# Performance work log

Measured on AMD Instinct MI355X. Metric: run time of the kernel, lower is better.

Reference implementation:

```python
import jax, jax.numpy as jnp
import numpy as np

B = 1048576  # batch size
D = 16       # in_dim == hid_dim == out_dim (required by the torch matmul broadcasting)


def setup_inputs() -> dict:
    key = jax.random.key(0)
    kx, kw = jax.random.split(key)
    x = jax.random.normal(kx, (B, D), dtype=jnp.float32)
    W = jax.random.normal(kw, (D, D, D), dtype=jnp.float32) * (1.0 / D)
    return {"x": x, "W": W}


def reference(x, W):
    # Original torch: xBx = x @ W @ x.T permuted, then take the batch diagonal.
    # Mathematically: out[b, k] = sum_{i, j} x[b, i] * W[k, i, j] * x[b, j]
    # (batched bilinear/quadratic form per output channel k). We compute only
    # the needed diagonal terms instead of the full BxB cross-batch product.
    return jnp.einsum('bi,kij,bj->bk', x, W, x)
```

## Files before the change

### kernel.cpp

```cpp
#include <hip/hip_runtime.h>
#include <hip/hip_bf16.h>


typedef __attribute__((ext_vector_type(8)))  short  short8;
typedef __attribute__((ext_vector_type(8)))  __bf16 bf16x8;
typedef __attribute__((ext_vector_type(4)))  float  floatx4;

#define DEV static __device__ __forceinline__

constexpr int cA(int c) {
    if (c < 24) { const int dIdx = c >> 1, v = c & 1;
        const int hi = dIdx / 3, lo = dIdx % 3 + 1;
        const int base = (hi == 3) ? 1 : 0;
        const int l = v ? ((lo == 1) ? 2 : 1) : 0;
        return base * 4 + l; }
    if (c < 36) { const int g = c - 24, hi = g / 4 + 1, l = g & 3;
        const int base = (hi == 3) ? 1 : 0;
        return base * 4 + l; }
    return c - 36;
}
constexpr int cDd(int c) {
    if (c < 24) { const int dIdx = c >> 1;
        return (dIdx / 3) * 4 + (dIdx % 3 + 1); }
    if (c < 36) { return ((c - 24) / 4 + 1) * 4; }
    return 0;
}
constexpr int   cB(int c) { return cA(c) ^ cDd(c); }
constexpr float cW(int c) { return (c >= 24 && c < 36) ? 0.5f : 1.0f; }

template <int C>
DEV float pval(const float* xv) {
    return xv[cA(C)] * xv[cB(C)];
}

template <int S>
DEV short8 make_afrag(const float* xv) {
    union { short8 s; __hip_bfloat162 h[4]; } u;
    u.h[0] = __float22bfloat162_rn(make_float2(pval<8 * S + 0>(xv), pval<8 * S + 1>(xv)));
    u.h[1] = __float22bfloat162_rn(make_float2(pval<8 * S + 2>(xv), pval<8 * S + 3>(xv)));
    u.h[2] = __float22bfloat162_rn(make_float2(pval<8 * S + 4>(xv), pval<8 * S + 5>(xv)));
    u.h[3] = __float22bfloat162_rn(make_float2(pval<8 * S + 6>(xv), pval<8 * S + 7>(xv)));
    return u.s;
}

DEV floatx4 mfma_bf16(short8 a, short8 b, floatx4 c) {
    return __builtin_amdgcn_mfma_f32_16x16x32_bf16(
        __builtin_bit_cast(bf16x8, a), __builtin_bit_cast(bf16x8, b), c, 0, 0, 0);
}

DEV float q_elem(const float* __restrict__ W, int e) {
    const int n = e / 160;
    const int k = e - n * 160;
    const int s = k >> 5, q = (k >> 3) & 3, j = k & 7;
    const int c = 8 * s + j;
    const int I = cA(c) ^ (q << 2);
    const int J = cB(c) ^ (q << 2);
    return (I == J) ? W[n * 256 + I * 16 + I]
                    : cW(c) * (W[n * 256 + I * 16 + J] + W[n * 256 + J * 16 + I]);
}

__global__ __launch_bounds__(256, 8)
void bilinear16_kernel(const float* __restrict__ x, const float* __restrict__ W,
                       float* __restrict__ out, int ntiles) {
    __shared__ __align__(16) short Qt[16][160];
    __shared__ __align__(16) float Tb[4][320];

    const int tid = threadIdx.x;
    for (int e = tid; e < 16 * 160; e += 256) {
        __hip_bfloat16 h = __float2bfloat16(q_elem(W, e));
        Qt[0][e] = *reinterpret_cast<short*>(&h);
    }
    __syncthreads();

    const int lane = tid & 63;
    const int n    = lane & 15;
    const int q    = lane >> 4;
    float* const tb = Tb[tid >> 6];

    short8 b0 = *reinterpret_cast<const short8*>(&Qt[n][0 * 32 + q * 8]);
    short8 b1 = *reinterpret_cast<const short8*>(&Qt[n][1 * 32 + q * 8]);
    short8 b2 = *reinterpret_cast<const short8*>(&Qt[n][2 * 32 + q * 8]);
    short8 b3 = *reinterpret_cast<const short8*>(&Qt[n][3 * 32 + q * 8]);
    short8 b4 = *reinterpret_cast<const short8*>(&Qt[n][4 * 32 + q * 8]);
    asm("" : "+a"(b0));
    asm("" : "+a"(b1));
    asm("" : "+a"(b2));
    asm("" : "+a"(b3));
    asm("" : "+a"(b4));

    const int waveId = blockIdx.x * 4 + (tid >> 6);
    const int nwaves = gridDim.x * 4;

    for (int t = waveId; t < ntiles; t += nwaves) {
        const float4 own = *reinterpret_cast<const float4*>(
            x + (size_t)t * 256 + n * 16 + q * 4);
        float4 s1, s2;
        s1.x = __shfl_xor(own.x, 16); s1.y = __shfl_xor(own.y, 16);
        s1.z = __shfl_xor(own.z, 16); s1.w = __shfl_xor(own.w, 16);
        s2.x = __shfl_xor(own.x, 32); s2.y = __shfl_xor(own.y, 32);
        s2.z = __shfl_xor(own.z, 32); s2.w = __shfl_xor(own.w, 32);
        const float xv[12] = {own.x, own.y, own.z, own.w,
                              s1.x,  s1.y,  s1.z,  s1.w,
                              s2.x,  s2.y,  s2.z,  s2.w};

        floatx4 acc0 = {0.f, 0.f, 0.f, 0.f};
        floatx4 acc1 = {0.f, 0.f, 0.f, 0.f};
        acc0 = mfma_bf16(make_afrag<0>(xv), b0, acc0);
        acc1 = mfma_bf16(make_afrag<1>(xv), b1, acc1);
        acc0 = mfma_bf16(make_afrag<2>(xv), b2, acc0);
        acc1 = mfma_bf16(make_afrag<3>(xv), b3, acc1);
        acc0 = mfma_bf16(make_afrag<4>(xv), b4, acc0);
        acc0 = acc0 + acc1;

        tb[(q * 4 + 0) * 20 + n] = acc0[0];
        tb[(q * 4 + 1) * 20 + n] = acc0[1];
        tb[(q * 4 + 2) * 20 + n] = acc0[2];
        tb[(q * 4 + 3) * 20 + n] = acc0[3];
        const float4 o = *reinterpret_cast<const float4*>(
            &tb[(lane >> 2) * 20 + (lane & 3) * 4]);
        *reinterpret_cast<float4*>(out + (size_t)t * 256 + lane * 4) = o;
    }
}

extern "C" void kernel_launch(void* const* d_in, const int* in_sizes, int n_in,
                              void* d_out, int out_size, void* d_ws, size_t ws_size,
                              hipStream_t stream) {
    const float* x = (const float*)d_in[0];
    const float* W = (const float*)d_in[1];
    float* out = (float*)d_out;
    const int Bn = in_sizes[0] / 16;
    const int ntiles = Bn >> 4;
    bilinear16_kernel<<<2048, 256, 0, stream>>>(x, W, out, ntiles);
}
```

Baseline: 122.9 us.

## Double-buffer x tiles into LDS via async global_load_lds prefetch

Adds a per-wave two-slot LDS ring filled with global_load_lds direct-to-LDS loads, so the loads for tile t+2 are in flight while tile t is computed. The loop is fully unrolled for the case of exactly 8 tiles per wave, which matches the default size (65536 tiles, 8192 waves). The ring also replaces the cross-lane shuffles: each lane reads its neighbours' x values straight from LDS. This is meant to hide global load latency in a memory-bound kernel, at the cost of extra LDS usage, manual vmcnt waits and a specialised code path that only fires when the tile count matches exactly.

```diff
diff --git a/kernel.cpp b/kernel.cpp
--- a/kernel.cpp
+++ b/kernel.cpp
@@ -59,11 +59,15 @@
                     : cW(c) * (W[n * 256 + I * 16 + J] + W[n * 256 + J * 16 + I]);
 }
 
+typedef const __attribute__((address_space(1))) unsigned char* gptr_t;
+typedef       __attribute__((address_space(3))) unsigned char* lptr_t;
+
 __global__ __launch_bounds__(256, 8)
 void bilinear16_kernel(const float* __restrict__ x, const float* __restrict__ W,
                        float* __restrict__ out, int ntiles) {
     __shared__ __align__(16) short Qt[16][160];
     __shared__ __align__(16) float Tb[4][320];
+    __shared__ __align__(16) float Ring[4][2][256];
 
     const int tid = threadIdx.x;
     for (int e = tid; e < 16 * 160; e += 256) {
@@ -75,34 +79,29 @@
     const int lane = tid & 63;
     const int n    = lane & 15;
     const int q    = lane >> 4;
-    float* const tb = Tb[tid >> 6];
+    const int wid  = tid >> 6;
+    float* const tb   = Tb[wid];
+    float* const ring = &Ring[wid][0][0];
 
     short8 b0 = *reinterpret_cast<const short8*>(&Qt[n][0 * 32 + q * 8]);
     short8 b1 = *reinterpret_cast<const short8*>(&Qt[n][1 * 32 + q * 8]);
     short8 b2 = *reinterpret_cast<const short8*>(&Qt[n][2 * 32 + q * 8]);
     short8 b3 = *reinterpret_cast<const short8*>(&Qt[n][3 * 32 + q * 8]);
     short8 b4 = *reinterpret_cast<const short8*>(&Qt[n][4 * 32 + q * 8]);
-    asm("" : "+a"(b0));
-    asm("" : "+a"(b1));
-    asm("" : "+a"(b2));
-    asm("" : "+a"(b3));
-    asm("" : "+a"(b4));
+    asm("" : "+a"(b0)); asm("" : "+a"(b1)); asm("" : "+a"(b2));
+    asm("" : "+a"(b3)); asm("" : "+a"(b4));
 
-    const int waveId = blockIdx.x * 4 + (tid >> 6);
+    const int waveId = blockIdx.x * 4 + wid;
     const int nwaves = gridDim.x * 4;
+    const int n16    = n * 16;
 
-    for (int t = waveId; t < ntiles; t += nwaves) {
-        const float4 own = *reinterpret_cast<const float4*>(
-            x + (size_t)t * 256 + n * 16 + q * 4);
-        float4 s1, s2;
-        s1.x = __shfl_xor(own.x, 16); s1.y = __shfl_xor(own.y, 16);
-        s1.z = __shfl_xor(own.z, 16); s1.w = __shfl_xor(own.w, 16);
-        s2.x = __shfl_xor(own.x, 32); s2.y = __shfl_xor(own.y, 32);
-        s2.z = __shfl_xor(own.z, 32); s2.w = __shfl_xor(own.w, 32);
-        const float xv[12] = {own.x, own.y, own.z, own.w,
-                              s1.x,  s1.y,  s1.z,  s1.w,
-                              s2.x,  s2.y,  s2.z,  s2.w};
-
+    auto tile_compute = [&](const float* rs, float* obase) {
+        const float4 v0 = *reinterpret_cast<const float4*>(rs + n16 + q * 4);
+        const float4 v1 = *reinterpret_cast<const float4*>(rs + n16 + (q ^ 1) * 4);
+        const float4 v2 = *reinterpret_cast<const float4*>(rs + n16 + (q ^ 2) * 4);
+        const float xv[12] = {v0.x, v0.y, v0.z, v0.w,
+                              v1.x, v1.y, v1.z, v1.w,
+                              v2.x, v2.y, v2.z, v2.w};
         floatx4 acc0 = {0.f, 0.f, 0.f, 0.f};
         floatx4 acc1 = {0.f, 0.f, 0.f, 0.f};
         acc0 = mfma_bf16(make_afrag<0>(xv), b0, acc0);
@@ -111,15 +110,64 @@
         acc1 = mfma_bf16(make_afrag<3>(xv), b3, acc1);
         acc0 = mfma_bf16(make_afrag<4>(xv), b4, acc0);
         acc0 = acc0 + acc1;
-
         tb[(q * 4 + 0) * 20 + n] = acc0[0];
         tb[(q * 4 + 1) * 20 + n] = acc0[1];
         tb[(q * 4 + 2) * 20 + n] = acc0[2];
         tb[(q * 4 + 3) * 20 + n] = acc0[3];
         const float4 o = *reinterpret_cast<const float4*>(
             &tb[(lane >> 2) * 20 + (lane & 3) * 4]);
-        *reinterpret_cast<float4*>(out + (size_t)t * 256 + lane * 4) = o;
+        *reinterpret_cast<float4*>(obase + lane * 4) = o;
+    };
+
+#define PREF(J)                                                                 \
+    __builtin_amdgcn_global_load_lds(                                           \
+        (gptr_t)(const void*)(x + (size_t)(t0 + (J) * nwaves) * 256 + lane * 4),\
+        (lptr_t)(void*)(ring + ((J) & 1) * 256), 16, 0, 0)
+
+#define TILE(J, VMC)                                                            \
+    do {                                                                        \
+        asm volatile("s_waitcnt vmcnt(" #VMC ")" ::: "memory");                 \
+        tile_compute(ring + ((J) & 1) * 256,                                    \
+                     out + (size_t)(t0 + (J) * nwaves) * 256);                  \
+        if ((J) < 6) { asm volatile("" ::: "memory"); PREF((J) + 2); }          \
+    } while (0)
+
+    if (ntiles == nwaves * 8) {
+        const int t0 = waveId;
+        PREF(0); PREF(1);
+        TILE(0, 1); TILE(1, 2); TILE(2, 2); TILE(3, 2);
+        TILE(4, 2); TILE(5, 2); TILE(6, 2); TILE(7, 1);
+    } else {
+        for (int t = waveId; t < ntiles; t += nwaves) {
+            const float4 own = *reinterpret_cast<const float4*>(
+                x + (size_t)t * 256 + n * 16 + q * 4);
+            float4 s1, s2;
+            s1.x = __shfl_xor(own.x, 16); s1.y = __shfl_xor(own.y, 16);
+            s1.z = __shfl_xor(own.z, 16); s1.w = __shfl_xor(own.w, 16);
+            s2.x = __shfl_xor(own.x, 32); s2.y = __shfl_xor(own.y, 32);
+            s2.z = __shfl_xor(own.z, 32); s2.w = __shfl_xor(own.w, 32);
+            const float xv[12] = {own.x, own.y, own.z, own.w,
+                                  s1.x,  s1.y,  s1.z,  s1.w,
+                                  s2.x,  s2.y,  s2.z,  s2.w};
+            floatx4 acc0 = {0.f, 0.f, 0.f, 0.f};
+            floatx4 acc1 = {0.f, 0.f, 0.f, 0.f};
+            acc0 = mfma_bf16(make_afrag<0>(xv), b0, acc0);
+            acc1 = mfma_bf16(make_afrag<1>(xv), b1, acc1);
+            acc0 = mfma_bf16(make_afrag<2>(xv), b2, acc0);
+            acc1 = mfma_bf16(make_afrag<3>(xv), b3, acc1);
+            acc0 = mfma_bf16(make_afrag<4>(xv), b4, acc0);
+            acc0 = acc0 + acc1;
+            tb[(q * 4 + 0) * 20 + n] = acc0[0];
+            tb[(q * 4 + 1) * 20 + n] = acc0[1];
+            tb[(q * 4 + 2) * 20 + n] = acc0[2];
+            tb[(q * 4 + 3) * 20 + n] = acc0[3];
+            const float4 o = *reinterpret_cast<const float4*>(
+                &tb[(lane >> 2) * 20 + (lane & 3) * 4]);
+            *reinterpret_cast<float4*>(out + (size_t)t * 256 + lane * 4) = o;
+        }
     }
+#undef TILE
+#undef PREF
 }
 
 extern "C" void kernel_launch(void* const* d_in, const int* in_sizes, int n_in,
```

After: 124.2 us. Within noise of the previous version (+1.1%).
